# Performance work log

Measured on AMD Instinct MI355X. Metric: run time of the kernel, lower is better.

The kernel has to match this reference:

```python
import jax, jax.numpy as jnp
import numpy as np

B, S, H, D = 2, 8192, 16, 64
P = 8            # lsh_num_projs
BS = 256         # block_size
SAMP = 256       # sample_size


def _gray_perm(num_projs):
    # AngularLSH._unit_hamming_distance_array: maps bin ids to Gray-code order
    a = np.array([0, 1], dtype=np.int32)
    for _ in range(num_projs - 1):
        a = np.concatenate([a, np.flip(a) + a.shape[0]])
    return a

_PERM = jnp.asarray(_gray_perm(P))          # (2**P,)
_POW2 = jnp.asarray(2 ** np.arange(P), dtype=jnp.int32)


def setup_inputs() -> dict:
    rng = jax.random.key(0)
    k1, k2, k3, k4, k5 = jax.random.split(rng, 5)
    return {
        "query": jax.random.normal(k1, (B, S, H, D), jnp.float32),
        "key": jax.random.normal(k2, (B, S, H, D), jnp.float32),
        "value": jax.random.normal(k3, (B, S, H, D), jnp.float32),
        "proj_dir": jax.random.normal(k4, (D, P), jnp.float32),
        "sample_idx": jax.random.randint(k5, (B, H, SAMP), 0, S),
    }


def _lsh_hash(x, proj_dir):
    # x: (B,S,H,D) -> Gray-coded bucket ids (B,H,S)
    bits = (jnp.einsum("bshd,dp->bhsp", x, proj_dir) > 0).astype(jnp.int32)
    bins = (bits * _POW2).sum(-1)
    return _PERM[bins]


def _gather_seq(x, idx_bhs):
    # x: (B,S,H,...) gathered along seq by idx (B,H,S)
    idx = jnp.transpose(idx_bhs, (0, 2, 1))  # (B,S,H)
    if x.ndim == 4:
        idx = idx[..., None]
    return jnp.take_along_axis(x, idx, axis=1)


def reference(query, key, value, proj_dir, sample_idx):
    scale = 1.0 / float(np.sqrt(D))
    nb = S // BS

    # --- LSH sort of queries and keys (stable argsort over seq) ---
    q_sort = jnp.argsort(_lsh_hash(query, proj_dir), axis=2)   # (B,H,S)
    k_sort = jnp.argsort(_lsh_hash(key, proj_dir), axis=2)     # (B,H,S)

    q_s = _gather_seq(query, q_sort)   # (B,S,H,D)
    k_s = _gather_seq(key, k_sort)
    v_s = _gather_seq(value, k_sort)

    # --- block-diagonal attention in sorted order ---
    qb = q_s.reshape(B, nb, BS, H, D)
    kb = k_s.reshape(B, nb, BS, H, D)
    vb = v_s.reshape(B, nb, BS, H, D)
    s_blk = jnp.einsum("bnihd,bnjhd->bhnij", qb, kb) * scale   # (B,H,nb,BS,BS)
    lse_blk = jax.nn.logsumexp(s_blk, axis=-1)                 # (B,H,nb,BS)
    a_blk = jnp.einsum("bhnij,bnjhd->bnihd", jax.nn.softmax(s_blk, axis=-1), vb)
    a_blk = a_blk.reshape(B, S, H, D)                          # sorted order
    lse_blk = jnp.transpose(lse_blk, (0, 2, 3, 1)).reshape(B, S, H)

    # un-sort back to original query order
    q_inv = jnp.argsort(q_sort, axis=2)                        # inverse perm (B,H,S)
    a_blk = _gather_seq(a_blk, q_inv)                          # (B,S,H,D)
    lse_blk = _gather_seq(lse_blk, q_inv)                      # (B,S,H)

    # --- residual: uniform sampled-key attention with importance weight ---
    k_r = _gather_seq(key, sample_idx)                         # (B,SAMP,H,D)
    v_r = _gather_seq(value, sample_idx)
    s_r = jnp.einsum("bihd,bjhd->bhij", query, k_r) * scale    # (B,H,S,SAMP)
    lse_r = jax.nn.logsumexp(s_r, axis=-1) + jnp.log(S / SAMP) # (B,H,S)
    a_r = jnp.einsum("bhij,bjhd->bihd", jax.nn.softmax(s_r, axis=-1), v_r)
    lse_r = jnp.transpose(lse_r, (0, 2, 1))                    # (B,S,H)

    # --- combine block + residual estimates via log-sum-exp ---
    lse_t = jnp.logaddexp(lse_blk, lse_r)                      # (B,S,H)
    w_blk = jnp.exp(lse_blk - lse_t)[..., None]
    w_r = jnp.exp(lse_r - lse_t)[..., None]
    attn = a_blk * w_blk + a_r * w_r                           # (B,S,H,D)
    return attn
```

## Files before the change

kernel.cpp:

```cpp
#include <hip/hip_runtime.h>
#include <hip/hip_bf16.h>

#define B 2
#define S 8192
#define H 16
#define D 64
#define NB 32
#define BS 256
#define SAMP 256
#define BH (B*H)
#define BHS (B*H*S)
#define BSHD (B*S*H*D)
#define LOG32 3.4657359027997265f

typedef float f32x4 __attribute__((ext_vector_type(4)));
typedef short bf16x8 __attribute__((ext_vector_type(8)));

__device__ __forceinline__ unsigned short f2bf(float x) {
    unsigned int u = __builtin_bit_cast(unsigned int, x);
    u += 0x7fffu + ((u >> 16) & 1u);
    return (unsigned short)(u >> 16);
}
__device__ __forceinline__ unsigned int pack2(float a, float b) {
    return (unsigned int)f2bf(a) | ((unsigned int)f2bf(b) << 16);
}

__global__ __launch_bounds__(256) void k_prep(const float* __restrict__ q,
                                              const float* __restrict__ k,
                                              const float* __restrict__ v,
                                              const float* __restrict__ pd,
                                              int* __restrict__ hq,
                                              int* __restrict__ hk,
                                              unsigned short* __restrict__ qbf,
                                              unsigned short* __restrict__ kbf,
                                              unsigned short* __restrict__ vbf) {
    __shared__ float spd[D * 8];
    const int t = threadIdx.x;
    for (int i = t; i < D * 8; i += 256) spd[i] = pd[i];
    __syncthreads();

    const int sc = blockIdx.x & (NB - 1);
    const int bh = blockIdx.x >> 5;
    const int s  = sc * 256 + t;
    const int h  = bh & (H - 1), b = bh >> 4;
    const int base = ((b * S + s) * H + h) << 6;

    float dq[8], dk[8];
#pragma unroll
    for (int p = 0; p < 8; ++p) { dq[p] = 0.f; dk[p] = 0.f; }

#pragma unroll
    for (int i = 0; i < 8; ++i) {
        float4 x0 = ((const float4*)(q + base + i * 8))[0];
        float4 x1 = ((const float4*)(q + base + i * 8))[1];
        float4 y0 = ((const float4*)(k + base + i * 8))[0];
        float4 y1 = ((const float4*)(k + base + i * 8))[1];
#pragma unroll
        for (int p = 0; p < 8; ++p) {
            dq[p] += x0.x * spd[(8*i+0)*8+p] + x0.y * spd[(8*i+1)*8+p]
                   + x0.z * spd[(8*i+2)*8+p] + x0.w * spd[(8*i+3)*8+p]
                   + x1.x * spd[(8*i+4)*8+p] + x1.y * spd[(8*i+5)*8+p]
                   + x1.z * spd[(8*i+6)*8+p] + x1.w * spd[(8*i+7)*8+p];
            dk[p] += y0.x * spd[(8*i+0)*8+p] + y0.y * spd[(8*i+1)*8+p]
                   + y0.z * spd[(8*i+2)*8+p] + y0.w * spd[(8*i+3)*8+p]
                   + y1.x * spd[(8*i+4)*8+p] + y1.y * spd[(8*i+5)*8+p]
                   + y1.z * spd[(8*i+6)*8+p] + y1.w * spd[(8*i+7)*8+p];
        }
        uint4 uq, uk;
        uq.x = pack2(x0.x * 0.125f, x0.y * 0.125f);
        uq.y = pack2(x0.z * 0.125f, x0.w * 0.125f);
        uq.z = pack2(x1.x * 0.125f, x1.y * 0.125f);
        uq.w = pack2(x1.z * 0.125f, x1.w * 0.125f);
        uk.x = pack2(y0.x, y0.y); uk.y = pack2(y0.z, y0.w);
        uk.z = pack2(y1.x, y1.y); uk.w = pack2(y1.z, y1.w);
        *(uint4*)(qbf + base + i * 8) = uq;
        *(uint4*)(kbf + base + i * 8) = uk;

        float4 z0 = ((const float4*)(v + base + i * 8))[0];
        float4 z1 = ((const float4*)(v + base + i * 8))[1];
        uint4 uv;
        uv.x = pack2(z0.x, z0.y); uv.y = pack2(z0.z, z0.w);
        uv.z = pack2(z1.x, z1.y); uv.w = pack2(z1.z, z1.w);
        *(uint4*)(vbf + base + i * 8) = uv;
    }
    int bq = 0, bk = 0;
#pragma unroll
    for (int p = 0; p < 8; ++p) {
        bq |= (dq[p] > 0.f) ? (1 << p) : 0;
        bk |= (dk[p] > 0.f) ? (1 << p) : 0;
    }
    hq[bh * S + s] = bq ^ (bq >> 1);
    hk[bh * S + s] = bk ^ (bk >> 1);
}

#define SORT_NT 64
#define SORT_CH (S / SORT_NT)

__global__ __launch_bounds__(SORT_NT) void k_sort(const int* __restrict__ hq,
                                                  const int* __restrict__ hk,
                                                  int* __restrict__ qs,
                                                  int* __restrict__ ks) {
    __shared__ int hist[SORT_NT * 256];
    __shared__ int base[257];
    const int t  = threadIdx.x;
    const int bh = blockIdx.x & (BH - 1);
    const bool isQ = blockIdx.x < BH;
    const int* hp = (isQ ? hq : hk) + bh * S;
    int*       sp = (isQ ? qs : ks) + bh * S;

    for (int i = 0; i < 256; ++i) hist[t * 256 + i] = 0;
    __syncthreads();
    for (int i = 0; i < SORT_CH; ++i) hist[t * 256 + hp[t * SORT_CH + i]]++;
    __syncthreads();

    for (int bi = 0; bi < 4; ++bi) {
        const int bin = t * 4 + bi;
        int sum = 0;
        for (int tt = 0; tt < SORT_NT; ++tt) sum += hist[tt * 256 + bin];
        base[bin + 1] = sum;
    }
    __syncthreads();
    if (t == 0) {
        base[0] = 0;
        for (int i = 1; i <= 256; ++i) base[i] += base[i - 1];
    }
    __syncthreads();

    for (int bi = 0; bi < 4; ++bi) {
        const int bin = t * 4 + bi;
        int run = base[bin];
        for (int tt = 0; tt < SORT_NT; ++tt) {
            int c = hist[tt * 256 + bin];
            hist[tt * 256 + bin] = run;
            run += c;
        }
    }
    __syncthreads();

    for (int i = 0; i < SORT_CH; ++i) {
        const int s0  = t * SORT_CH + i;
        const int bin = hp[s0];
        sp[hist[t * 256 + bin]++] = s0;
    }
}

#define VP 264
#define PP 40

__global__ __launch_bounds__(512, 4) void k_attn(const unsigned short* __restrict__ qbf,
                                                 const unsigned short* __restrict__ kbf,
                                                 const unsigned short* __restrict__ vbf,
                                                 const int* __restrict__ qs,
                                                 const int* __restrict__ ks,
                                                 const int* __restrict__ sidx,
                                                 float* __restrict__ out) {
    __shared__ __align__(16) unsigned short vT[64 * VP];
    __shared__ __align__(16) unsigned short pL[8 * 32 * PP];

    const int t    = threadIdx.x;
    const int w    = t >> 6;
    const int lane = t & 63;
    const int lg   = lane >> 4;
    const int lr   = lane & 15;
    const int blk  = blockIdx.x & (NB - 1);
    const int bh   = blockIdx.x >> 5;
    const int h    = bh & (H - 1), b = bh >> 4;
    const int sbase = bh * S + blk * BS;
    unsigned short* pw = pL + w * 32 * PP;

    int qrow[2]; bf16x8 bq[2][2];
#pragma unroll
    for (int qg = 0; qg < 2; ++qg) {
        qrow[qg] = qs[sbase + w * 32 + qg * 16 + lr];
        const unsigned short* qp = qbf + (((b * S + qrow[qg]) * H + h) << 6);
        bq[qg][0] = *(const bf16x8*)(qp + lg * 8);
        bq[qg][1] = *(const bf16x8*)(qp + 32 + lg * 8);
    }

    float m_run[2] = {-1e30f, -1e30f}, l_run[2] = {0.f, 0.f};
    f32x4 acc[2][4];
#pragma unroll
    for (int qg = 0; qg < 2; ++qg)
#pragma unroll
        for (int dg = 0; dg < 4; ++dg) acc[qg][dg] = (f32x4){0.f, 0.f, 0.f, 0.f};

    for (int pass = 0; pass < 2; ++pass) {
        if (pass) __syncthreads();
        {
            const int key = t >> 1, d0 = (t & 1) * 32;
            const int krow = pass ? sidx[bh * SAMP + key] : ks[sbase + key];
            const unsigned short* vp = vbf + (((b * S + krow) * H + h) << 6) + d0;
#pragma unroll
            for (int i = 0; i < 4; ++i) {
                uint4 x = *(const uint4*)(vp + i * 8);
                const int d = d0 + i * 8;
                vT[(d + 0) * VP + key] = (unsigned short)(x.x);
                vT[(d + 1) * VP + key] = (unsigned short)(x.x >> 16);
                vT[(d + 2) * VP + key] = (unsigned short)(x.y);
                vT[(d + 3) * VP + key] = (unsigned short)(x.y >> 16);
                vT[(d + 4) * VP + key] = (unsigned short)(x.z);
                vT[(d + 5) * VP + key] = (unsigned short)(x.z >> 16);
                vT[(d + 6) * VP + key] = (unsigned short)(x.w);
                vT[(d + 7) * VP + key] = (unsigned short)(x.w >> 16);
            }
        }
        __syncthreads();

        const float bias = pass ? LOG32 : 0.f;
        for (int kt4 = 0; kt4 < 4; ++kt4) {
            int krw[4];
#pragma unroll
            for (int kg = 0; kg < 4; ++kg) {
                const int key = kt4 * 64 + kg * 16 + lr;
                krw[kg] = pass ? sidx[bh * SAMP + key] : ks[sbase + key];
            }
            f32x4 c[2][4];
#pragma unroll
            for (int kf = 0; kf < 2; ++kf) {
                bf16x8 ak[4];
#pragma unroll
                for (int kg = 0; kg < 4; ++kg)
                    ak[kg] = *(const bf16x8*)(kbf + (((b * S + krw[kg]) * H + h) << 6)
                                              + kf * 32 + lg * 8);
#pragma unroll
                for (int qg = 0; qg < 2; ++qg)
#pragma unroll
                    for (int kg = 0; kg < 4; ++kg) {
                        f32x4 cin = kf ? c[qg][kg] : (f32x4){0.f, 0.f, 0.f, 0.f};
                        c[qg][kg] = __builtin_amdgcn_mfma_f32_16x16x32_bf16(ak[kg], bq[qg][kf], cin, 0, 0, 0);
                    }
            }
            float esc[2];
#pragma unroll
            for (int qg = 0; qg < 2; ++qg) {
                float tm = -1e30f;
#pragma unroll
                for (int kg = 0; kg < 4; ++kg)
#pragma unroll
                    for (int r = 0; r < 4; ++r) tm = fmaxf(tm, c[qg][kg][r]);
                tm = fmaxf(tm, __shfl_xor(tm, 16));
                tm = fmaxf(tm, __shfl_xor(tm, 32));
                tm += bias;
                const float mn = fmaxf(m_run[qg], tm);
                esc[qg] = __expf(m_run[qg] - mn);
                m_run[qg] = mn;
                const float mnb = mn - bias;
                float rs = 0.f;
#pragma unroll
                for (int kg = 0; kg < 4; ++kg)
#pragma unroll
                    for (int r = 0; r < 4; ++r) {
                        const float p = __expf(c[qg][kg][r] - mnb);
                        c[qg][kg][r] = p;
                        rs += p;
                    }
                rs += __shfl_xor(rs, 16);
                rs += __shfl_xor(rs, 32);
                l_run[qg] = l_run[qg] * esc[qg] + rs;
            }
#pragma unroll
            for (int qg = 0; qg < 2; ++qg)
#pragma unroll
                for (int r = 0; r < 4; ++r) {
                    const float er = __shfl(esc[qg], lg * 4 + r);
#pragma unroll
                    for (int dg = 0; dg < 4; ++dg) acc[qg][dg][r] *= er;
                }
#pragma unroll
            for (int hh = 0; hh < 2; ++hh) {
#pragma unroll
                for (int qg = 0; qg < 2; ++qg)
#pragma unroll
                    for (int kg2 = 0; kg2 < 2; ++kg2) {
                        const int kg = hh * 2 + kg2;
                        uint2 u;
                        u.x = pack2(c[qg][kg][0], c[qg][kg][1]);
                        u.y = pack2(c[qg][kg][2], c[qg][kg][3]);
                        *(uint2*)&pw[(qg * 16 + lr) * PP + kg2 * 16 + lg * 4] = u;
                    }
                bf16x8 bv[4];
#pragma unroll
                for (int dg = 0; dg < 4; ++dg)
                    bv[dg] = *(const bf16x8*)&vT[(dg * 16 + lr) * VP + kt4 * 64 + hh * 32 + lg * 8];
#pragma unroll
                for (int qg = 0; qg < 2; ++qg) {
                    const bf16x8 ap = *(const bf16x8*)&pw[(qg * 16 + lr) * PP + lg * 8];
#pragma unroll
                    for (int dg = 0; dg < 4; ++dg)
                        acc[qg][dg] = __builtin_amdgcn_mfma_f32_16x16x32_bf16(ap, bv[dg], acc[qg][dg], 0, 0, 0);
                }
            }
        }
    }

#pragma unroll
    for (int qg = 0; qg < 2; ++qg)
#pragma unroll
        for (int r = 0; r < 4; ++r) {
            const float lq = __shfl(l_run[qg], lg * 4 + r);
            const int   qr = __shfl(qrow[qg], lg * 4 + r);
            const float inv = 1.f / lq;
            const int obase = ((b * S + qr) * H + h) << 6;
#pragma unroll
            for (int dg = 0; dg < 4; ++dg)
                out[obase + dg * 16 + lr] = acc[qg][dg][r] * inv;
        }
}

extern "C" void kernel_launch(void* const* d_in, const int* in_sizes, int n_in,
                              void* d_out, int out_size, void* d_ws, size_t ws_size,
                              hipStream_t stream) {
    const float* q   = (const float*)d_in[0];
    const float* k   = (const float*)d_in[1];
    const float* v   = (const float*)d_in[2];
    const float* pd  = (const float*)d_in[3];
    const int*  sidx = (const int*)d_in[4];
    float* out = (float*)d_out;

    int* hq = (int*)d_ws;
    int* hk = hq + BHS;
    int* qs = hk + BHS;
    int* ks = qs + BHS;
    unsigned short* qbf = (unsigned short*)(ks + BHS);
    unsigned short* kbf = qbf + BSHD;
    unsigned short* vbf = kbf + BSHD;

    k_prep<<<BH * NB, 256, 0, stream>>>(q, k, v, pd, hq, hk, qbf, kbf, vbf);
    k_sort<<<2 * BH, SORT_NT, 0, stream>>>(hq, hk, qs, ks);
    k_attn<<<BH * NB, 512, 0, stream>>>(qbf, kbf, vbf, qs, ks, sidx, out);
}
```

Measured before the change: 230.4 us.

## Drop bf16 staging copies; convert q/k/v to bf16 inside attention kernel

The prep kernel no longer writes bf16 copies of q, k and v. It only computes LSH hashes, and its thread mapping now makes each block cover 16 consecutive sequence positions across all heads, so reads are contiguous and hash writes are vectorized through shared memory. The attention kernel reads fp32 q/k/v directly and converts them to bf16 in registers, which removes a full write plus re-read of three bf16 tensors. In exchange, the attention kernel's gathered loads double in bytes, and K rows are re-read for the residual pass and across query tiles.

Result: slower. 286.2 us (+24.2%).

```diff
diff --git a/kernel.cpp b/kernel.cpp
--- a/kernel.cpp
+++ b/kernel.cpp
@@ -10,7 +10,6 @@
 #define SAMP 256
 #define BH (B*H)
 #define BHS (B*H*S)
-#define BSHD (B*S*H*D)
 #define LOG32 3.4657359027997265f
 
 typedef float f32x4 __attribute__((ext_vector_type(4)));
@@ -25,72 +24,56 @@
     return (unsigned int)f2bf(a) | ((unsigned int)f2bf(b) << 16);
 }
 
-__global__ __launch_bounds__(256) void k_prep(const float* __restrict__ q,
+__device__ __forceinline__ int hash_row(const float* __restrict__ rp,
+                                        const float* __restrict__ spd) {
+    float d[8];
+#pragma unroll
+    for (int p = 0; p < 8; ++p) d[p] = 0.f;
+#pragma unroll
+    for (int i = 0; i < 8; ++i) {
+        float4 x0 = ((const float4*)(rp + i * 8))[0];
+        float4 x1 = ((const float4*)(rp + i * 8))[1];
+#pragma unroll
+        for (int p = 0; p < 8; ++p) {
+            d[p] += x0.x * spd[(8*i+0)*8+p] + x0.y * spd[(8*i+1)*8+p]
+                  + x0.z * spd[(8*i+2)*8+p] + x0.w * spd[(8*i+3)*8+p]
+                  + x1.x * spd[(8*i+4)*8+p] + x1.y * spd[(8*i+5)*8+p]
+                  + x1.z * spd[(8*i+6)*8+p] + x1.w * spd[(8*i+7)*8+p];
+        }
+    }
+    int bits = 0;
+#pragma unroll
+    for (int p = 0; p < 8; ++p) bits |= (d[p] > 0.f) ? (1 << p) : 0;
+    return bits ^ (bits >> 1);
+}
+
+__global__ __launch_bounds__(256) void k_hash(const float* __restrict__ q,
                                               const float* __restrict__ k,
-                                              const float* __restrict__ v,
                                               const float* __restrict__ pd,
                                               int* __restrict__ hq,
-                                              int* __restrict__ hk,
-                                              unsigned short* __restrict__ qbf,
-                                              unsigned short* __restrict__ kbf,
-                                              unsigned short* __restrict__ vbf) {
+                                              int* __restrict__ hk) {
     __shared__ float spd[D * 8];
+    __shared__ int   ht[2][16][16];
     const int t = threadIdx.x;
     for (int i = t; i < D * 8; i += 256) spd[i] = pd[i];
     __syncthreads();
 
-    const int sc = blockIdx.x & (NB - 1);
-    const int bh = blockIdx.x >> 5;
-    const int s  = sc * 256 + t;
-    const int h  = bh & (H - 1), b = bh >> 4;
-    const int base = ((b * S + s) * H + h) << 6;
-
-    float dq[8], dk[8];
-#pragma unroll
-    for (int p = 0; p < 8; ++p) { dq[p] = 0.f; dk[p] = 0.f; }
-
-#pragma unroll
-    for (int i = 0; i < 8; ++i) {
-        float4 x0 = ((const float4*)(q + base + i * 8))[0];
-        float4 x1 = ((const float4*)(q + base + i * 8))[1];
-        float4 y0 = ((const float4*)(k + base + i * 8))[0];
-        float4 y1 = ((const float4*)(k + base + i * 8))[1];
-#pragma unroll
-        for (int p = 0; p < 8; ++p) {
-            dq[p] += x0.x * spd[(8*i+0)*8+p] + x0.y * spd[(8*i+1)*8+p]
-                   + x0.z * spd[(8*i+2)*8+p] + x0.w * spd[(8*i+3)*8+p]
-                   + x1.x * spd[(8*i+4)*8+p] + x1.y * spd[(8*i+5)*8+p]
-                   + x1.z * spd[(8*i+6)*8+p] + x1.w * spd[(8*i+7)*8+p];
-            dk[p] += y0.x * spd[(8*i+0)*8+p] + y0.y * spd[(8*i+1)*8+p]
-                   + y0.z * spd[(8*i+2)*8+p] + y0.w * spd[(8*i+3)*8+p]
-                   + y1.x * spd[(8*i+4)*8+p] + y1.y * spd[(8*i+5)*8+p]
-                   + y1.z * spd[(8*i+6)*8+p] + y1.w * spd[(8*i+7)*8+p];
-        }
-        uint4 uq, uk;
-        uq.x = pack2(x0.x * 0.125f, x0.y * 0.125f);
-        uq.y = pack2(x0.z * 0.125f, x0.w * 0.125f);
-        uq.z = pack2(x1.x * 0.125f, x1.y * 0.125f);
-        uq.w = pack2(x1.z * 0.125f, x1.w * 0.125f);
-        uk.x = pack2(y0.x, y0.y); uk.y = pack2(y0.z, y0.w);
-        uk.z = pack2(y1.x, y1.y); uk.w = pack2(y1.z, y1.w);
-        *(uint4*)(qbf + base + i * 8) = uq;
-        *(uint4*)(kbf + base + i * 8) = uk;
-
-        float4 z0 = ((const float4*)(v + base + i * 8))[0];
-        float4 z1 = ((const float4*)(v + base + i * 8))[1];
-        uint4 uv;
-        uv.x = pack2(z0.x, z0.y); uv.y = pack2(z0.z, z0.w);
-        uv.z = pack2(z1.x, z1.y); uv.w = pack2(z1.z, z1.w);
-        *(uint4*)(vbf + base + i * 8) = uv;
-    }
-    int bq = 0, bk = 0;
-#pragma unroll
-    for (int p = 0; p < 8; ++p) {
-        bq |= (dq[p] > 0.f) ? (1 << p) : 0;
-        bk |= (dk[p] > 0.f) ? (1 << p) : 0;
-    }
-    hq[bh * S + s] = bq ^ (bq >> 1);
-    hk[bh * S + s] = bk ^ (bk >> 1);
+    const int b  = blockIdx.x >> 9;
+    const int s0 = (blockIdx.x & 511) * 16;
+    const int sl = t >> 4;
+    const int h  = t & 15;
+    const int base = ((b * S + s0 + sl) * H + h) * D;
+
+    ht[0][h][sl] = hash_row(q + base, spd);
+    ht[1][h][sl] = hash_row(k + base, spd);
+    __syncthreads();
+
+    if (t < 128) {
+        const int inp = t >> 6, r = t & 63, h2 = r >> 2, p2 = r & 3;
+        int4 val = *(const int4*)&ht[inp][h2][p2 * 4];
+        int* dst = inp ? hk : hq;
+        *(int4*)&dst[(b * H + h2) * S + s0 + p2 * 4] = val;
+    }
 }
 
 #define SORT_NT 64
@@ -147,9 +130,9 @@
 #define VP 264
 #define PP 40
 
-__global__ __launch_bounds__(512, 4) void k_attn(const unsigned short* __restrict__ qbf,
-                                                 const unsigned short* __restrict__ kbf,
-                                                 const unsigned short* __restrict__ vbf,
+__global__ __launch_bounds__(512, 4) void k_attn(const float* __restrict__ q,
+                                                 const float* __restrict__ k,
+                                                 const float* __restrict__ v,
                                                  const int* __restrict__ qs,
                                                  const int* __restrict__ ks,
                                                  const int* __restrict__ sidx,
@@ -172,9 +155,18 @@
 #pragma unroll
     for (int qg = 0; qg < 2; ++qg) {
         qrow[qg] = qs[sbase + w * 32 + qg * 16 + lr];
-        const unsigned short* qp = qbf + (((b * S + qrow[qg]) * H + h) << 6);
-        bq[qg][0] = *(const bf16x8*)(qp + lg * 8);
-        bq[qg][1] = *(const bf16x8*)(qp + 32 + lg * 8);
+        const float* qp = q + (((b * S + qrow[qg]) * H + h) << 6);
+#pragma unroll
+        for (int kf = 0; kf < 2; ++kf) {
+            float4 x0 = ((const float4*)(qp + kf * 32 + lg * 8))[0];
+            float4 x1 = ((const float4*)(qp + kf * 32 + lg * 8))[1];
+            union { bf16x8 v8; unsigned int u[4]; } fa;
+            fa.u[0] = pack2(x0.x * 0.125f, x0.y * 0.125f);
+            fa.u[1] = pack2(x0.z * 0.125f, x0.w * 0.125f);
+            fa.u[2] = pack2(x1.x * 0.125f, x1.y * 0.125f);
+            fa.u[3] = pack2(x1.z * 0.125f, x1.w * 0.125f);
+            bq[qg][kf] = fa.v8;
+        }
     }
 
     float m_run[2] = {-1e30f, -1e30f}, l_run[2] = {0.f, 0.f};
@@ -189,19 +181,20 @@
         {
             const int key = t >> 1, d0 = (t & 1) * 32;
             const int krow = pass ? sidx[bh * SAMP + key] : ks[sbase + key];
-            const unsigned short* vp = vbf + (((b * S + krow) * H + h) << 6) + d0;
+            const float* vp = v + (((b * S + krow) * H + h) << 6) + d0;
 #pragma unroll
             for (int i = 0; i < 4; ++i) {
-                uint4 x = *(const uint4*)(vp + i * 8);
+                float4 y0 = ((const float4*)(vp + i * 8))[0];
+                float4 y1 = ((const float4*)(vp + i * 8))[1];
                 const int d = d0 + i * 8;
-                vT[(d + 0) * VP + key] = (unsigned short)(x.x);
-                vT[(d + 1) * VP + key] = (unsigned short)(x.x >> 16);
-                vT[(d + 2) * VP + key] = (unsigned short)(x.y);
-                vT[(d + 3) * VP + key] = (unsigned short)(x.y >> 16);
-                vT[(d + 4) * VP + key] = (unsigned short)(x.z);
-                vT[(d + 5) * VP + key] = (unsigned short)(x.z >> 16);
-                vT[(d + 6) * VP + key] = (unsigned short)(x.w);
-                vT[(d + 7) * VP + key] = (unsigned short)(x.w >> 16);
+                vT[(d + 0) * VP + key] = f2bf(y0.x);
+                vT[(d + 1) * VP + key] = f2bf(y0.y);
+                vT[(d + 2) * VP + key] = f2bf(y0.z);
+                vT[(d + 3) * VP + key] = f2bf(y0.w);
+                vT[(d + 4) * VP + key] = f2bf(y1.x);
+                vT[(d + 5) * VP + key] = f2bf(y1.y);
+                vT[(d + 6) * VP + key] = f2bf(y1.z);
+                vT[(d + 7) * VP + key] = f2bf(y1.w);
             }
         }
         __syncthreads();
@@ -217,11 +210,24 @@
             f32x4 c[2][4];
 #pragma unroll
             for (int kf = 0; kf < 2; ++kf) {
+                float4 xr[4][2];
+#pragma unroll
+                for (int kg = 0; kg < 4; ++kg) {
+                    const float* kr = k + (((b * S + krw[kg]) * H + h) << 6)
+                                      + kf * 32 + lg * 8;
+                    xr[kg][0] = ((const float4*)kr)[0];
+                    xr[kg][1] = ((const float4*)kr)[1];
+                }
                 bf16x8 ak[4];
 #pragma unroll
-                for (int kg = 0; kg < 4; ++kg)
-                    ak[kg] = *(const bf16x8*)(kbf + (((b * S + krw[kg]) * H + h) << 6)
-                                              + kf * 32 + lg * 8);
+                for (int kg = 0; kg < 4; ++kg) {
+                    union { bf16x8 v8; unsigned int u[4]; } fb;
+                    fb.u[0] = pack2(xr[kg][0].x, xr[kg][0].y);
+                    fb.u[1] = pack2(xr[kg][0].z, xr[kg][0].w);
+                    fb.u[2] = pack2(xr[kg][1].x, xr[kg][1].y);
+                    fb.u[3] = pack2(xr[kg][1].z, xr[kg][1].w);
+                    ak[kg] = fb.v8;
+                }
 #pragma unroll
                 for (int qg = 0; qg < 2; ++qg)
 #pragma unroll
@@ -321,11 +327,8 @@
     int* hk = hq + BHS;
     int* qs = hk + BHS;
     int* ks = qs + BHS;
-    unsigned short* qbf = (unsigned short*)(ks + BHS);
-    unsigned short* kbf = qbf + BSHD;
-    unsigned short* vbf = kbf + BSHD;
-
-    k_prep<<<BH * NB, 256, 0, stream>>>(q, k, v, pd, hq, hk, qbf, kbf, vbf);
+
+    k_hash<<<B * (S / 16), 256, 0, stream>>>(q, k, pd, hq, hk);
     k_sort<<<2 * BH, SORT_NT, 0, stream>>>(hq, hk, qs, ks);
-    k_attn<<<BH * NB, 512, 0, stream>>>(qbf, kbf, vbf, qs, ks, sidx, out);
-}
+    k_attn<<<BH * NB, 512, 0, stream>>>(q, k, v, qs, ks, sidx, out);
+}
```

## Coalesce prep loads across heads and remap attention blocks across XCDs

Applied to the files above, without the earlier changes.

The prep kernel now gives each block 16 consecutive sequence positions across all 16 heads, so a warp's loads cover contiguous (s,h,d) memory rather than stride-H rows. Hash bits go through shared memory and are written out as vectorized int4 stores in the (b,h,s) layout. Q, K and V are handled one after another to lower register pressure. The attention kernel also permutes block ids so consecutive logical blocks of one head land on the same XCD, which should improve L2 locality for the shared sampled keys.

Result: slower. 467.6 us (+102.9%).

```diff
diff --git a/kernel.cpp b/kernel.cpp
--- a/kernel.cpp
+++ b/kernel.cpp
@@ -35,62 +35,86 @@
                                               unsigned short* __restrict__ kbf,
                                               unsigned short* __restrict__ vbf) {
     __shared__ float spd[D * 8];
+    __shared__ int   ht[2][16][16];
     const int t = threadIdx.x;
     for (int i = t; i < D * 8; i += 256) spd[i] = pd[i];
     __syncthreads();
 
-    const int sc = blockIdx.x & (NB - 1);
-    const int bh = blockIdx.x >> 5;
-    const int s  = sc * 256 + t;
-    const int h  = bh & (H - 1), b = bh >> 4;
-    const int base = ((b * S + s) * H + h) << 6;
-
-    float dq[8], dk[8];
-#pragma unroll
-    for (int p = 0; p < 8; ++p) { dq[p] = 0.f; dk[p] = 0.f; }
-
+    const int b  = blockIdx.x >> 9;
+    const int s0 = (blockIdx.x & 511) * 16;
+    const int sl = t >> 4;
+    const int h  = t & 15;
+    const int base = ((b * S + s0 + sl) * H + h) << 6;
+
+    {
+        float d[8];
+#pragma unroll
+        for (int p = 0; p < 8; ++p) d[p] = 0.f;
+#pragma unroll
+        for (int i = 0; i < 8; ++i) {
+            float4 x0 = ((const float4*)(q + base + i * 8))[0];
+            float4 x1 = ((const float4*)(q + base + i * 8))[1];
+#pragma unroll
+            for (int p = 0; p < 8; ++p) {
+                d[p] += x0.x * spd[(8*i+0)*8+p] + x0.y * spd[(8*i+1)*8+p]
+                      + x0.z * spd[(8*i+2)*8+p] + x0.w * spd[(8*i+3)*8+p]
+                      + x1.x * spd[(8*i+4)*8+p] + x1.y * spd[(8*i+5)*8+p]
+                      + x1.z * spd[(8*i+6)*8+p] + x1.w * spd[(8*i+7)*8+p];
+            }
+            uint4 u;
+            u.x = pack2(x0.x * 0.125f, x0.y * 0.125f);
+            u.y = pack2(x0.z * 0.125f, x0.w * 0.125f);
+            u.z = pack2(x1.x * 0.125f, x1.y * 0.125f);
+            u.w = pack2(x1.z * 0.125f, x1.w * 0.125f);
+            *(uint4*)(qbf + base + i * 8) = u;
+        }
+        int bits = 0;
+#pragma unroll
+        for (int p = 0; p < 8; ++p) bits |= (d[p] > 0.f) ? (1 << p) : 0;
+        ht[0][h][sl] = bits ^ (bits >> 1);
+    }
+    {
+        float d[8];
+#pragma unroll
+        for (int p = 0; p < 8; ++p) d[p] = 0.f;
+#pragma unroll
+        for (int i = 0; i < 8; ++i) {
+            float4 x0 = ((const float4*)(k + base + i * 8))[0];
+            float4 x1 = ((const float4*)(k + base + i * 8))[1];
+#pragma unroll
+            for (int p = 0; p < 8; ++p) {
+                d[p] += x0.x * spd[(8*i+0)*8+p] + x0.y * spd[(8*i+1)*8+p]
+                      + x0.z * spd[(8*i+2)*8+p] + x0.w * spd[(8*i+3)*8+p]
+                      + x1.x * spd[(8*i+4)*8+p] + x1.y * spd[(8*i+5)*8+p]
+                      + x1.z * spd[(8*i+6)*8+p] + x1.w * spd[(8*i+7)*8+p];
+            }
+            uint4 u;
+            u.x = pack2(x0.x, x0.y); u.y = pack2(x0.z, x0.w);
+            u.z = pack2(x1.x, x1.y); u.w = pack2(x1.z, x1.w);
+            *(uint4*)(kbf + base + i * 8) = u;
+        }
+        int bits = 0;
+#pragma unroll
+        for (int p = 0; p < 8; ++p) bits |= (d[p] > 0.f) ? (1 << p) : 0;
+        ht[1][h][sl] = bits ^ (bits >> 1);
+    }
 #pragma unroll
     for (int i = 0; i < 8; ++i) {
-        float4 x0 = ((const float4*)(q + base + i * 8))[0];
-        float4 x1 = ((const float4*)(q + base + i * 8))[1];
-        float4 y0 = ((const float4*)(k + base + i * 8))[0];
-        float4 y1 = ((const float4*)(k + base + i * 8))[1];
-#pragma unroll
-        for (int p = 0; p < 8; ++p) {
-            dq[p] += x0.x * spd[(8*i+0)*8+p] + x0.y * spd[(8*i+1)*8+p]
-                   + x0.z * spd[(8*i+2)*8+p] + x0.w * spd[(8*i+3)*8+p]
-                   + x1.x * spd[(8*i+4)*8+p] + x1.y * spd[(8*i+5)*8+p]
-                   + x1.z * spd[(8*i+6)*8+p] + x1.w * spd[(8*i+7)*8+p];
-            dk[p] += y0.x * spd[(8*i+0)*8+p] + y0.y * spd[(8*i+1)*8+p]
-                   + y0.z * spd[(8*i+2)*8+p] + y0.w * spd[(8*i+3)*8+p]
-                   + y1.x * spd[(8*i+4)*8+p] + y1.y * spd[(8*i+5)*8+p]
-                   + y1.z * spd[(8*i+6)*8+p] + y1.w * spd[(8*i+7)*8+p];
-        }
-        uint4 uq, uk;
-        uq.x = pack2(x0.x * 0.125f, x0.y * 0.125f);
-        uq.y = pack2(x0.z * 0.125f, x0.w * 0.125f);
-        uq.z = pack2(x1.x * 0.125f, x1.y * 0.125f);
-        uq.w = pack2(x1.z * 0.125f, x1.w * 0.125f);
-        uk.x = pack2(y0.x, y0.y); uk.y = pack2(y0.z, y0.w);
-        uk.z = pack2(y1.x, y1.y); uk.w = pack2(y1.z, y1.w);
-        *(uint4*)(qbf + base + i * 8) = uq;
-        *(uint4*)(kbf + base + i * 8) = uk;
-
-        float4 z0 = ((const float4*)(v + base + i * 8))[0];
-        float4 z1 = ((const float4*)(v + base + i * 8))[1];
-        uint4 uv;
-        uv.x = pack2(z0.x, z0.y); uv.y = pack2(z0.z, z0.w);
-        uv.z = pack2(z1.x, z1.y); uv.w = pack2(z1.z, z1.w);
-        *(uint4*)(vbf + base + i * 8) = uv;
-    }
-    int bq = 0, bk = 0;
-#pragma unroll
-    for (int p = 0; p < 8; ++p) {
-        bq |= (dq[p] > 0.f) ? (1 << p) : 0;
-        bk |= (dk[p] > 0.f) ? (1 << p) : 0;
-    }
-    hq[bh * S + s] = bq ^ (bq >> 1);
-    hk[bh * S + s] = bk ^ (bk >> 1);
+        float4 x0 = ((const float4*)(v + base + i * 8))[0];
+        float4 x1 = ((const float4*)(v + base + i * 8))[1];
+        uint4 u;
+        u.x = pack2(x0.x, x0.y); u.y = pack2(x0.z, x0.w);
+        u.z = pack2(x1.x, x1.y); u.w = pack2(x1.z, x1.w);
+        *(uint4*)(vbf + base + i * 8) = u;
+    }
+    __syncthreads();
+
+    if (t < 128) {
+        const int inp = t >> 6, r = t & 63, h2 = r >> 2, p2 = r & 3;
+        int4 val = *(const int4*)&ht[inp][h2][p2 * 4];
+        int* dst = inp ? hk : hq;
+        *(int4*)&dst[(b * H + h2) * S + s0 + p2 * 4] = val;
+    }
 }
 
 #define SORT_NT 64
@@ -162,8 +186,9 @@
     const int lane = t & 63;
     const int lg   = lane >> 4;
     const int lr   = lane & 15;
-    const int blk  = blockIdx.x & (NB - 1);
-    const int bh   = blockIdx.x >> 5;
+    const int logical = (blockIdx.x & 7) * (BH * NB / 8) + (blockIdx.x >> 3);
+    const int blk  = logical & (NB - 1);
+    const int bh   = logical >> 5;
     const int h    = bh & (H - 1), b = bh >> 4;
     const int sbase = bh * S + blk * BS;
     unsigned short* pw = pL + w * 32 * PP;
@@ -325,7 +350,7 @@
     unsigned short* kbf = qbf + BSHD;
     unsigned short* vbf = kbf + BSHD;
 
-    k_prep<<<BH * NB, 256, 0, stream>>>(q, k, v, pd, hq, hk, qbf, kbf, vbf);
+    k_prep<<<B * (S / 16), 256, 0, stream>>>(q, k, v, pd, hq, hk, qbf, kbf, vbf);
     k_sort<<<2 * BH, SORT_NT, 0, stream>>>(hq, hk, qs, ks);
     k_attn<<<BH * NB, 512, 0, stream>>>(qbf, kbf, vbf, qs, ks, sidx, out);
 }
```
